# Kernel optimization log

Hardware: AMD Instinct MI355X
Metric: run time of the kernel (lower is better)

## Reference

```python
import jax, jax.numpy as jnp
import numpy as np

B, T, D, H, d = 2, 2048, 1024, 16, 64
INNER = H * d
SCALE = d ** -0.5


def _rope(x, inv_freq):
    # x: [B, H, T, d], interleaved rotary as in the torch module
    t = x.shape[2]
    pos = jnp.arange(t, dtype=jnp.float32)
    freqs = pos[:, None] * inv_freq[None, :]          # [T, d/2]
    cos_f, sin_f = jnp.cos(freqs), jnp.sin(freqs)
    x1, x2 = x[..., 0::2], x[..., 1::2]
    y1 = x1 * cos_f - x2 * sin_f
    y2 = x1 * sin_f + x2 * cos_f
    return jnp.stack([y1, y2], axis=-1).reshape(x.shape)


def setup_inputs() -> dict:
    key = jax.random.key(0)
    ks = jax.random.split(key, 6)
    x = jax.random.normal(ks[0], (B, T, D), jnp.float32)
    W_qkv = jax.random.normal(ks[1], (D, 3 * INNER), jnp.float32) * (D ** -0.5)
    W_out = jax.random.normal(ks[2], (INNER, D), jnp.float32) * (INNER ** -0.5)
    W_dt = jax.random.normal(ks[3], (D, H), jnp.float32) * 0.01
    b_dt = jnp.full((H,), -4.0, jnp.float32)
    W_gsp = jax.random.normal(ks[4], (D, INNER), jnp.float32) * 0.01
    b_gsp = jnp.full((INNER,), -3.0, jnp.float32)
    inv_freq = 1.0 / (10000.0 ** (jnp.arange(0, d, 2, dtype=jnp.float32) / d))
    return {"x": x, "W_qkv": W_qkv, "W_out": W_out, "W_dt": W_dt,
            "b_dt": b_dt, "W_gsp": W_gsp, "b_gsp": b_gsp, "inv_freq": inv_freq}


def reference(x, W_qkv, W_out, W_dt, b_dt, W_gsp, b_gsp, inv_freq):
    qkv = (x @ W_qkv).reshape(B, T, 3, H, d)
    Q = jnp.moveaxis(qkv[:, :, 0], 1, 2)   # [B,H,T,d]
    K = jnp.moveaxis(qkv[:, :, 1], 1, 2)
    V = jnp.moveaxis(qkv[:, :, 2], 1, 2)
    Q = _rope(Q, inv_freq)
    K = _rope(K, inv_freq)

    dt = jax.nn.softplus(x @ W_dt + b_dt)             # [B,T,H]
    gamma = jnp.moveaxis(jnp.exp(-dt), 1, 2)          # [B,H,T]

    p = jax.nn.sigmoid(x @ W_gsp + b_gsp).reshape(B, T, H, d)
    p = jnp.moveaxis(p, 1, 2)                          # [B,H,T,d]
    gamma_eff = gamma[..., None] * (1.0 - p) + p
    gamma_scalar = gamma_eff.mean(axis=-1)            # [B,H,T]
    V = V * (1.0 - p)

    log_gamma = jnp.log(jnp.clip(gamma_scalar, 1e-6, 1.0 - 1e-6))
    lgc = jnp.cumsum(log_gamma, axis=-1)              # [B,H,T]
    log_D = jnp.clip(lgc[..., :, None] - lgc[..., None, :], -20.0, 0.0)
    causal = jnp.tril(jnp.ones((T, T), jnp.float32))
    Dm = jnp.exp(log_D) * causal                      # [B,H,T,T]

    Wscore = jnp.einsum('bhtd,bhsd->bhts', Q * SCALE, K)
    A = Wscore * Dm
    Y = jnp.einsum('bhts,bhsd->bhtd', A, V)
    Y = jnp.moveaxis(Y, 1, 2).reshape(B, T, INNER)
    return Y @ W_out
```

## Files before the change

kernel.cpp:

```cpp
#include <hip/hip_runtime.h>
#include <hip/hip_bf16.h>
#include <math.h>

#define B_     2
#define T_     2048
#define D_     1024
#define H_     16
#define INNER_ 1024
#define NC_    4096
#define SCALE_ 0.125f

typedef unsigned short u16;
typedef short short8 __attribute__((ext_vector_type(8)));
typedef float f32x4 __attribute__((ext_vector_type(4)));
typedef float f32x16 __attribute__((ext_vector_type(16)));
typedef unsigned short u16x4 __attribute__((ext_vector_type(4)));
typedef unsigned int u32x2 __attribute__((ext_vector_type(2)));

__device__ __forceinline__ u16 f2bf(float x) {
  union { float f; unsigned u; } v; v.f = x;
  unsigned r = v.u + 0x7fffu + ((v.u >> 16) & 1u);
  return (u16)(r >> 16);
}
__device__ __forceinline__ float b2f(u16 x) {
  union { unsigned u; float f; } v; v.u = ((unsigned)x) << 16;
  return v.f;
}
__device__ __forceinline__ unsigned cvtpk(float lo, float hi) {
  unsigned r;
  asm("v_cvt_pk_bf16_f32 %0, %1, %2" : "=v"(r) : "v"(lo), "v"(hi));
  return r;
}
__device__ __forceinline__ void gload16(const void* g, void* l) {
  __builtin_amdgcn_global_load_lds(
      (const __attribute__((address_space(1))) void*)g,
      (__attribute__((address_space(3))) void*)l, 16, 0, 0);
}

__global__ __launch_bounds__(256) void prep_kernel(
    const float* __restrict__ x, const float* __restrict__ W_qkv,
    const float* __restrict__ W_gsp, const float* __restrict__ W_out,
    const float* __restrict__ W_dt, const float* __restrict__ inv_freq,
    u16* __restrict__ xb, u16* __restrict__ Wcombt, u16* __restrict__ Woutt,
    u16* __restrict__ Wdtb, float2* __restrict__ tab) {
  const int bid = blockIdx.x, tid = threadIdx.x;
  if (bid < 1280) {
    const float* src; u16* dst; int N, nx, ky;
    if (bid < 768)       { src = W_qkv; dst = Wcombt;                N = 3072; nx = bid % 48;          ky = bid / 48; }
    else if (bid < 1024) { src = W_gsp; dst = Wcombt + 3072 * 1024;  N = 1024; nx = (bid - 768) % 16;  ky = (bid - 768) / 16; }
    else                 { src = W_out; dst = Woutt;                 N = 1024; nx = (bid - 1024) % 16; ky = (bid - 1024) / 16; }
    __shared__ float tile[64][65];
    const int k0 = ky * 64, n0 = nx * 64;
    for (int e = tid; e < 4096; e += 256) {
      int kk = e >> 6, nn = e & 63;
      tile[kk][nn] = src[(size_t)(k0 + kk) * N + n0 + nn];
    }
    __syncthreads();
    for (int e = tid; e < 4096; e += 256) {
      int nn = e >> 6, kk = e & 63;
      dst[(size_t)(n0 + nn) * 1024 + k0 + kk] = f2bf(tile[kk][nn]);
    }
  } else if (bid < 1344) {
    int i = (bid - 1280) * 256 + tid;
    int k = i >> 4, h = i & 15;
    Wdtb[(size_t)h * D_ + k] = f2bf(W_dt[i]);
  } else if (bid < 1600) {
    int i = (bid - 1344) * 256 + tid;
    int t = i >> 5, j = i & 31;
    float s, c;
    sincosf((float)t * inv_freq[j], &s, &c);
    tab[i] = make_float2(c, s);
  } else {
    int base = (bid - 1600) * 1024 + tid;
#pragma unroll
    for (int r = 0; r < 4; ++r) {
      int i = base + r * 256;
      float4 v = *reinterpret_cast<const float4*>(x + (size_t)i * 4);
      u16x4 o; o.x = f2bf(v.x); o.y = f2bf(v.y); o.z = f2bf(v.z); o.w = f2bf(v.w);
      *reinterpret_cast<u16x4*>(xb + (size_t)i * 4) = o;
    }
  }
}

__global__ __launch_bounds__(256, 2) void gemm_big(
    const u16* __restrict__ A, const u16* __restrict__ Bt,
    u16* __restrict__ C) {
  __shared__ u16 As[2][128 * 32] __attribute__((aligned(16)));
  __shared__ u16 Bs[2][256 * 32] __attribute__((aligned(16)));
  const int tid = threadIdx.x;
  const int w = tid >> 6, l = tid & 63;
  const int bid = blockIdx.x;
  const int xcd = bid & 7, idx = bid >> 3;
  const int brow = xcd * 4 + (idx & 3);
  const int bcol = idx >> 2;
  const int m0 = brow * 128, n0 = bcol * 256;
  const int ql = l & 15, g4 = l >> 4;
  const int srow = tid >> 2;
  const int ssl  = (tid & 3) ^ (srow & 3);

  const u16* Ag = A + (size_t)m0 * D_;
  const u16* Bg = Bt + (size_t)n0 * D_;

  auto STAGE = [&](int kt, int bp) {
#pragma unroll
    for (int c = 0; c < 2; ++c)
      gload16(Ag + (size_t)(c * 64 + srow) * D_ + kt * 32 + ssl * 8,
              (char*)As[bp] + c * 4096 + tid * 16);
#pragma unroll
    for (int c = 0; c < 4; ++c)
      gload16(Bg + (size_t)(c * 64 + srow) * D_ + kt * 32 + ssl * 8,
              (char*)Bs[bp] + c * 4096 + tid * 16);
  };

  f32x4 acc[8][4] = {};
  STAGE(0, 0);

  const int NT = D_ / 32;
  for (int kt = 0; kt < NT; ++kt) {
    const int bp = kt & 1;
    asm volatile("s_waitcnt vmcnt(0)" ::: "memory");
    __builtin_amdgcn_sched_barrier(0);
    __builtin_amdgcn_s_barrier();
    __builtin_amdgcn_sched_barrier(0);
    if (kt + 1 < NT) STAGE(kt + 1, bp ^ 1);

    const char* Asb = (const char*)As[bp];
    const char* Bsb = (const char*)Bs[bp];
    short8 bf[4], af[4];
#pragma unroll
    for (int nf = 0; nf < 4; ++nf) {
      int row = w * 64 + nf * 16 + ql;
      bf[nf] = *(const short8*)(Bsb + row * 64 + ((g4 ^ (row & 3)) << 4));
    }
#pragma unroll
    for (int mf = 0; mf < 4; ++mf) {
      int row = mf * 16 + ql;
      af[mf] = *(const short8*)(Asb + row * 64 + ((g4 ^ (row & 3)) << 4));
    }
    __builtin_amdgcn_s_setprio(1);
#pragma unroll
    for (int mf = 0; mf < 4; ++mf)
#pragma unroll
      for (int nf = 0; nf < 4; ++nf)
        acc[mf][nf] = __builtin_amdgcn_mfma_f32_16x16x32_bf16(af[mf], bf[nf], acc[mf][nf], 0, 0, 0);
    __builtin_amdgcn_s_setprio(0);
#pragma unroll
    for (int mf = 0; mf < 4; ++mf) {
      int row = 64 + mf * 16 + ql;
      af[mf] = *(const short8*)(Asb + row * 64 + ((g4 ^ (row & 3)) << 4));
    }
    __builtin_amdgcn_s_setprio(1);
#pragma unroll
    for (int mf = 0; mf < 4; ++mf)
#pragma unroll
      for (int nf = 0; nf < 4; ++nf)
        acc[mf + 4][nf] = __builtin_amdgcn_mfma_f32_16x16x32_bf16(af[mf], bf[nf], acc[mf + 4][nf], 0, 0, 0);
    __builtin_amdgcn_s_setprio(0);
  }

#pragma unroll
  for (int mf = 0; mf < 8; ++mf) {
#pragma unroll
    for (int r = 0; r < 4; ++r) {
      size_t row = (size_t)(m0 + mf * 16 + g4 * 4 + r);
      size_t base = row * NC_ + n0 + w * 64 + ql;
#pragma unroll
      for (int nf = 0; nf < 4; ++nf)
        C[base + nf * 16] = f2bf(acc[mf][nf][r]);
    }
  }
}

template <bool BF16OUT>
__global__ __launch_bounds__(256) void gemm_bt(
    const u16* __restrict__ A, const u16* __restrict__ Bt,
    void* __restrict__ Cv, int M, int N, int K) {
  __shared__ u16 As[2][128 * 64] __attribute__((aligned(16)));
  __shared__ u16 Bs[2][128 * 64] __attribute__((aligned(16)));
  const int tid = threadIdx.x, w = tid >> 6, l = tid & 63;
  const int rpx = (M >> 7) >> 3;
  const int bid = blockIdx.x;
  const int xcd = bid & 7, idx = bid >> 3;
  const int brow = xcd * rpx + (idx % rpx);
  const int bcol = idx / rpx;
  const int m0 = brow * 128, n0 = bcol * 128;
  const int wr = (w >> 1) * 64, wc = (w & 1) * 64;
  const int srow = l >> 3;
  const int kgrp = ((l & 7) ^ srow) * 8;

  f32x4 acc[4][4] = {};

  auto stage = [&](int kt, int bs) {
#pragma unroll
    for (int i = 0; i < 4; ++i) {
      int c = w * 4 + i;
      int row = c * 8 + srow;
      gload16(A + (size_t)(m0 + row) * K + kt * 64 + kgrp, (char*)As[bs] + c * 1024);
      gload16(Bt + (size_t)(n0 + row) * K + kt * 64 + kgrp, (char*)Bs[bs] + c * 1024);
    }
  };

  stage(0, 0);
  const int NT = K >> 6;
  for (int kt = 0; kt < NT; ++kt) {
    asm volatile("s_waitcnt vmcnt(0)" ::: "memory");
    __builtin_amdgcn_sched_barrier(0);
    __builtin_amdgcn_s_barrier();
    __builtin_amdgcn_sched_barrier(0);
    if (kt + 1 < NT) stage(kt + 1, (kt + 1) & 1);

    const char* Asb = (const char*)As[kt & 1];
    const char* Bsb = (const char*)Bs[kt & 1];
#pragma unroll
    for (int kk = 0; kk < 2; ++kk) {
      short8 af[4], bf[4];
#pragma unroll
      for (int i = 0; i < 4; ++i) {
        int ra = wr + i * 16 + (l & 15);
        int sa = kk * 4 + (l >> 4);
        af[i] = *(const short8*)(Asb + ra * 128 + ((sa ^ (ra & 7)) << 4));
        int rb = wc + i * 16 + (l & 15);
        bf[i] = *(const short8*)(Bsb + rb * 128 + ((sa ^ (rb & 7)) << 4));
      }
#pragma unroll
      for (int i = 0; i < 4; ++i)
#pragma unroll
        for (int j = 0; j < 4; ++j)
          acc[i][j] = __builtin_amdgcn_mfma_f32_16x16x32_bf16(af[i], bf[j], acc[i][j], 0, 0, 0);
    }
  }
#pragma unroll
  for (int i = 0; i < 4; ++i) {
#pragma unroll
    for (int r = 0; r < 4; ++r) {
      size_t row = (size_t)(m0 + wr + i * 16 + (l >> 4) * 4 + r);
      size_t base = row * N + n0 + wc + (l & 15);
#pragma unroll
      for (int j = 0; j < 4; ++j) {
        if (BF16OUT) ((u16*)Cv)[base + j * 16] = f2bf(acc[i][j][r]);
        else         ((float*)Cv)[base + j * 16] = acc[i][j][r];
      }
    }
  }
}

__global__ __launch_bounds__(256) void pointwise_kernel(
    const u16* __restrict__ C, const u16* __restrict__ xb,
    const u16* __restrict__ Wdtb, const float* __restrict__ b_dt,
    const float* __restrict__ b_gsp, const float2* __restrict__ tab,
    u16* __restrict__ Qb, u16* __restrict__ Kb, u16* __restrict__ Vb,
    float* __restrict__ lg) {
  const int row = blockIdx.x * 4 + (threadIdx.x >> 6);
  const int l = threadIdx.x & 63;
  const int b = row >> 11, t = row & (T_ - 1);
  const int h = l >> 2;
  const int dd0 = (l & 3) * 16;
  const int col = h * 64 + dd0;
  const size_t cb = (size_t)row * NC_;

  float gsum = 0.f;
  {
    const int kc = (l & 3) * 256;
    const short8* xpg = (const short8*)(xb + (size_t)row * D_ + kc);
    const short8* wpg = (const short8*)(Wdtb + h * D_ + kc);
#pragma unroll
    for (int i = 0; i < 32; ++i) {
      short8 xv = xpg[i], wv = wpg[i];
#pragma unroll
      for (int j = 0; j < 8; ++j) gsum += b2f((u16)xv[j]) * b2f((u16)wv[j]);
    }
    gsum += __shfl_xor(gsum, 1);
    gsum += __shfl_xor(gsum, 2);
  }
  const float dtv = gsum + b_dt[h];
  const float sp = (dtv > 20.f) ? dtv : log1pf(__expf(dtv));
  const float gh = __expf(-sp);

  const short8* qp = (const short8*)(C + cb + col);
  const short8* kp = (const short8*)(C + cb + 1024 + col);
  const short8* vp = (const short8*)(C + cb + 2048 + col);
  const short8* pp = (const short8*)(C + cb + 3072 + col);
  short8 q0 = qp[0], q1 = qp[1];
  short8 k0 = kp[0], k1 = kp[1];
  short8 v0 = vp[0], v1 = vp[1];
  short8 pr0 = pp[0], pr1 = pp[1];

  float ge = 0.f;
  short8 vo0, vo1;
#pragma unroll
  for (int i = 0; i < 8; ++i) {
    float pv = b2f((u16)pr0[i]) + b_gsp[col + i];
    float p = 1.f / (1.f + __expf(-pv));
    ge += gh * (1.f - p) + p;
    vo0[i] = (short)f2bf(b2f((u16)v0[i]) * (1.f - p));
    float pv1 = b2f((u16)pr1[i]) + b_gsp[col + 8 + i];
    float p1 = 1.f / (1.f + __expf(-pv1));
    ge += gh * (1.f - p1) + p1;
    vo1[i] = (short)f2bf(b2f((u16)v1[i]) * (1.f - p1));
  }
  const size_t hm = (((size_t)(b * H_ + h)) * T_ + t) * 64 + dd0;
  ((short8*)(Vb + hm))[0] = vo0;
  ((short8*)(Vb + hm))[1] = vo1;

  ge += __shfl_xor(ge, 1);
  ge += __shfl_xor(ge, 2);
  if ((l & 3) == 0) {
    float gs = ge * (1.f / 64.f);
    gs = fminf(fmaxf(gs, 1e-6f), 1.f - 1e-6f);
    lg[((size_t)(b * H_ + h)) * T_ + t] = logf(gs);
  }

  short8 qo0, qo1, ko0, ko1;
  const float2* cs = tab + t * 32 + (dd0 >> 1);
#pragma unroll
  for (int m = 0; m < 4; ++m) {
    float2 c0 = cs[m];
    float qa = b2f((u16)q0[2 * m]), qb = b2f((u16)q0[2 * m + 1]);
    qo0[2 * m]     = (short)f2bf((qa * c0.x - qb * c0.y) * SCALE_);
    qo0[2 * m + 1] = (short)f2bf((qa * c0.y + qb * c0.x) * SCALE_);
    float ka = b2f((u16)k0[2 * m]), kb = b2f((u16)k0[2 * m + 1]);
    ko0[2 * m]     = (short)f2bf(ka * c0.x - kb * c0.y);
    ko0[2 * m + 1] = (short)f2bf(ka * c0.y + kb * c0.x);
    float2 c1 = cs[4 + m];
    float qa1 = b2f((u16)q1[2 * m]), qb1 = b2f((u16)q1[2 * m + 1]);
    qo1[2 * m]     = (short)f2bf((qa1 * c1.x - qb1 * c1.y) * SCALE_);
    qo1[2 * m + 1] = (short)f2bf((qa1 * c1.y + qb1 * c1.x) * SCALE_);
    float ka1 = b2f((u16)k1[2 * m]), kb1 = b2f((u16)k1[2 * m + 1]);
    ko1[2 * m]     = (short)f2bf(ka1 * c1.x - kb1 * c1.y);
    ko1[2 * m + 1] = (short)f2bf(ka1 * c1.y + kb1 * c1.x);
  }
  ((short8*)(Qb + hm))[0] = qo0; ((short8*)(Qb + hm))[1] = qo1;
  ((short8*)(Kb + hm))[0] = ko0; ((short8*)(Kb + hm))[1] = ko1;
}

__global__ __launch_bounds__(256) void scan_kernel(
    const float* __restrict__ lg, float* __restrict__ lgc) {
  const size_t base = (size_t)blockIdx.x * T_;
  const int tid = threadIdx.x;
  __shared__ float sums[256];
  float loc[8];
  float run = 0.f;
#pragma unroll
  for (int i = 0; i < 8; ++i) { run += lg[base + tid * 8 + i]; loc[i] = run; }
  sums[tid] = run;
  __syncthreads();
  if (tid == 0) {
    float r = 0.f;
    for (int i = 0; i < 256; ++i) { float v = sums[i]; sums[i] = r; r += v; }
  }
  __syncthreads();
  const float off = sums[tid];
#pragma unroll
  for (int i = 0; i < 8; ++i) lgc[base + tid * 8 + i] = off + loc[i];
}

__global__ __launch_bounds__(256) void kv_prep_kernel(
    const u16* __restrict__ Vb, const float* __restrict__ lgc,
    u16* __restrict__ Vtg) {
  const int stile = blockIdx.x;
  const int bh = blockIdx.y;
  const int tid = threadIdx.x;
  __shared__ u16 vt[64][72];
  const size_t base = ((size_t)bh * T_ + (size_t)stile * 64) * 64;
  const float* lgp = lgc + (size_t)bh * T_;
  const float lgb = lgp[stile * 64];
#pragma unroll
  for (int i = 0; i < 2; ++i) {
    int c = tid * 2 + i;
    int row = c >> 3, k8 = (c & 7) * 8;
    float beta = __expf(lgb - lgp[stile * 64 + row]);
    short8 vv = *(const short8*)(Vb + base + row * 64 + k8);
#pragma unroll
    for (int j = 0; j < 8; ++j) vt[row][k8 + j] = f2bf(b2f((u16)vv[j]) * beta);
  }
  __syncthreads();
#pragma unroll
  for (int i = 0; i < 2; ++i) {
    int c = tid * 2 + i;
    int dd = c >> 3, t8 = (c & 7) * 8;
    short8 o;
#pragma unroll
    for (int j = 0; j < 8; ++j) o[j] = (short)vt[t8 + j][dd];
    *(short8*)(Vtg + ((size_t)(bh * 32 + stile) * 64 + dd) * 64 + t8) = o;
  }
}

__global__ __launch_bounds__(256) void attn_mfma(
    const u16* __restrict__ Qb, const u16* __restrict__ Kb,
    const u16* __restrict__ Vtg, const float* __restrict__ lgc,
    u16* __restrict__ Y) {
  const int i = blockIdx.x;
  const int xcd = i & 7;
  const int half = i >> 8;
  const int r = (i >> 3) & 31;
  const int q8 = r >> 2;
  const int bh_hi = r & 3;
  const int qb = half ? (15 - q8) : q8;
  const int bh = xcd + (bh_hi << 3);
  const int b = bh >> 4, h = bh & 15;
  const int tid = threadIdx.x, w = tid >> 6, l = tid & 63;
  const int l31 = l & 31, hi = l >> 5;
  __shared__ u16 Ks[3][64 * 64] __attribute__((aligned(16)));
  __shared__ u16 Vs[3][64 * 64] __attribute__((aligned(16)));
  const u16* Qg = Qb + (size_t)bh * T_ * 64;
  const u16* Kg = Kb + (size_t)bh * T_ * 64;
  const u16* Vg = Vtg + (size_t)bh * 32 * 4096;
  const float* lgp = lgc + (size_t)bh * T_;
  const int srow = l >> 3, slot8 = l & 7;

  const int q0 = qb * 128 + w * 32;
  const int qg = q0 + l31;
  short8 qf[4];
#pragma unroll
  for (int kk = 0; kk < 4; ++kk)
    qf[kk] = *(const short8*)(Qg + (size_t)qg * 64 + kk * 16 + hi * 8);
  const float lgq = lgp[qg];
  const float lgtop = lgp[qb * 128];

  f32x16 yacc0 = {}, yacc1 = {};

  const int st0 = qb * 2 + 1;
  int s_min;
  {
    int lo = 0, hic = st0;
    while (lo < hic) {
      int mid = (lo + hic) >> 1;
      if (lgtop - lgp[mid * 64 + 63] > -20.f) hic = mid; else lo = mid + 1;
    }
    s_min = lo;
  }

  auto STAGE = [&](int s) {
    const int bs = s % 3;
#pragma unroll
    for (int i2 = 0; i2 < 2; ++i2) {
      int c = w * 2 + i2, row = c * 8 + srow;
      int kg = (slot8 ^ (row & 7)) * 8;
      gload16(Kg + (size_t)(s * 64 + row) * 64 + kg, (char*)Ks[bs] + c * 1024);
      gload16(Vg + (size_t)s * 4096 + row * 64 + kg, (char*)Vs[bs] + c * 1024);
    }
  };

  STAGE(st0);
  if (st0 - 1 >= s_min) STAGE(st0 - 1);

  for (int st = st0; st >= s_min; --st) {
    if (st - 1 >= s_min) asm volatile("s_waitcnt vmcnt(4)" ::: "memory");
    else                 asm volatile("s_waitcnt vmcnt(0)" ::: "memory");
    __builtin_amdgcn_sched_barrier(0);
    __builtin_amdgcn_s_barrier();
    __builtin_amdgcn_sched_barrier(0);
    if (st - 2 >= s_min) STAGE(st - 2);

    const bool allinv = (st * 64 > q0 + 31);
    if (!allinv) {
      const int bs = st % 3;
      const char* Ksb = (const char*)Ks[bs];
      const char* Vsb = (const char*)Vs[bs];
      const float alpha = __expf(lgq - lgp[st * 64]);
      const bool domask = (st * 64 + 63 > q0);
      const int qrel = qg - st * 64;
#pragma unroll
      for (int sblk = 0; sblk < 2; ++sblk) {
        f32x16 c = {};
        __builtin_amdgcn_s_setprio(1);
#pragma unroll
        for (int kk = 0; kk < 4; ++kk) {
          int row = sblk * 32 + l31;
          short8 kf = *(const short8*)(Ksb + row * 128 + (((kk * 2 + hi) ^ (row & 7)) << 4));
          c = __builtin_amdgcn_mfma_f32_32x32x16_bf16(kf, qf[kk], c, 0, 0, 0);
        }
        __builtin_amdgcn_s_setprio(0);
        float pv[16];
#pragma unroll
        for (int ii = 0; ii < 16; ++ii) {
          float p = c[ii] * alpha;
          if (domask) {
            int s64 = sblk * 32 + (ii & 3) + 8 * (ii >> 2) + 4 * hi;
            if (s64 > qrel) p = 0.f;
          }
          pv[ii] = p;
        }
        unsigned A0 = cvtpk(pv[0], pv[1]),  A1 = cvtpk(pv[2], pv[3]);
        unsigned B0 = cvtpk(pv[4], pv[5]),  B1 = cvtpk(pv[6], pv[7]);
        u32x2 ra = __builtin_amdgcn_permlane32_swap(A0, B0, false, false);
        u32x2 rb = __builtin_amdgcn_permlane32_swap(A1, B1, false, false);
        unsigned C0 = cvtpk(pv[8], pv[9]),  C1 = cvtpk(pv[10], pv[11]);
        unsigned D0 = cvtpk(pv[12], pv[13]), D1 = cvtpk(pv[14], pv[15]);
        u32x2 rc = __builtin_amdgcn_permlane32_swap(C0, D0, false, false);
        u32x2 rd = __builtin_amdgcn_permlane32_swap(C1, D1, false, false);
        union { unsigned u[4]; short8 s; } f0, f1;
        f0.u[0] = ra[0]; f0.u[1] = rb[0]; f0.u[2] = ra[1]; f0.u[3] = rb[1];
        f1.u[0] = rc[0]; f1.u[1] = rd[0]; f1.u[2] = rc[1]; f1.u[3] = rd[1];
#pragma unroll
        for (int fi = 0; fi < 2; ++fi) {
          const short8 pf = fi ? f1.s : f0.s;
          const int kkg = sblk * 2 + fi;
          short8 vf0 = *(const short8*)(Vsb + l31 * 128 + (((kkg * 2 + hi) ^ (l31 & 7)) << 4));
          short8 vf1 = *(const short8*)(Vsb + (32 + l31) * 128 + (((kkg * 2 + hi) ^ (l31 & 7)) << 4));
          __builtin_amdgcn_s_setprio(1);
          yacc0 = __builtin_amdgcn_mfma_f32_32x32x16_bf16(pf, vf0, yacc0, 0, 0, 0);
          yacc1 = __builtin_amdgcn_mfma_f32_32x32x16_bf16(pf, vf1, yacc1, 0, 0, 0);
          __builtin_amdgcn_s_setprio(0);
        }
      }
    }
  }

#pragma unroll
  for (int reg = 0; reg < 16; ++reg) {
    int qrow = (reg & 3) + 8 * (reg >> 2) + 4 * hi;
    size_t rowg = (size_t)(b * T_) + qb * 128 + w * 32 + qrow;
    Y[rowg * INNER_ + h * 64 + l31] = f2bf(yacc0[reg]);
    Y[rowg * INNER_ + h * 64 + 32 + l31] = f2bf(yacc1[reg]);
  }
}

extern "C" void kernel_launch(void* const* d_in, const int* in_sizes, int n_in,
                              void* d_out, int out_size, void* d_ws, size_t ws_size,
                              hipStream_t stream) {
  const float* x        = (const float*)d_in[0];
  const float* W_qkv    = (const float*)d_in[1];
  const float* W_out    = (const float*)d_in[2];
  const float* W_dt     = (const float*)d_in[3];
  const float* b_dt     = (const float*)d_in[4];
  const float* W_gsp    = (const float*)d_in[5];
  const float* b_gsp    = (const float*)d_in[6];
  const float* inv_freq = (const float*)d_in[7];
  float* out = (float*)d_out;

  const int M = B_ * T_;
  char* p = (char*)d_ws;
  auto alloc = [&](size_t bytes) {
    char* r = p; p += (bytes + 255) & ~(size_t)255; return r;
  };
  u16*    xb    = (u16*)alloc((size_t)M * D_ * 2);
  u16*    Wcombt= (u16*)alloc((size_t)NC_ * D_ * 2);
  u16*    Woutt = (u16*)alloc((size_t)D_ * INNER_ * 2);
  u16*    Wdtb  = (u16*)alloc((size_t)H_ * D_ * 2);
  u16*    Cqkvp = (u16*)alloc((size_t)M * NC_ * 2);
  u16*    Qb    = (u16*)alloc((size_t)B_ * H_ * T_ * 64 * 2);
  u16*    Kb    = (u16*)alloc((size_t)B_ * H_ * T_ * 64 * 2);
  u16*    Vb    = (u16*)alloc((size_t)B_ * H_ * T_ * 64 * 2);
  float*  lg    = (float*)alloc((size_t)B_ * H_ * T_ * 4);
  float*  lgc   = (float*)alloc((size_t)B_ * H_ * T_ * 4);
  float2* tab   = (float2*)alloc((size_t)T_ * 32 * 8);
  u16*    Vtg   = Cqkvp;
  u16*    Yb    = Cqkvp + (size_t)4 * 1024 * 1024;

  prep_kernel<<<2624, 256, 0, stream>>>(x, W_qkv, W_gsp, W_out, W_dt, inv_freq,
                                        xb, Wcombt, Woutt, Wdtb, tab);
  gemm_big<<<512, 256, 0, stream>>>(xb, Wcombt, Cqkvp);

  pointwise_kernel<<<M / 4, 256, 0, stream>>>(Cqkvp, xb, Wdtb, b_dt, b_gsp,
                                              tab, Qb, Kb, Vb, lg);
  scan_kernel<<<B_ * H_, 256, 0, stream>>>(lg, lgc);
  kv_prep_kernel<<<dim3(T_ / 64, B_ * H_), 256, 0, stream>>>(Vb, lgc, Vtg);

  attn_mfma<<<512, 256, 0, stream>>>(Qb, Kb, Vtg, lgc, Yb);

  gemm_bt<false><<<256, 256, 0, stream>>>(Yb, Woutt, out, M, D_, INNER_);
}
```

Measured before the change: 150.6 us.

## Restructure attention into 512-thread blocks with 256-row query tiles and split-S reduction

The attention kernel now runs 256 blocks of 512 threads. Each block covers 256 query rows, and each wave handles 64 query rows over half of each 64-key tile. The two key halves are combined at the end through an LDS reduction. This reuses K fragments across two query sub-tiles and halves the number of K/V tile loads per query, but it drops the old reversed query-block ordering used for causal load balancing and adds barriers and a reduction step. Per-block work is now more uneven and fewer blocks are in flight.

```diff
diff --git a/kernel.cpp b/kernel.cpp
--- a/kernel.cpp
+++ b/kernel.cpp
@@ -385,41 +385,40 @@
   }
 }
 
-__global__ __launch_bounds__(256) void attn_mfma(
+__global__ __launch_bounds__(512) void attn_mfma(
     const u16* __restrict__ Qb, const u16* __restrict__ Kb,
     const u16* __restrict__ Vtg, const float* __restrict__ lgc,
     u16* __restrict__ Y) {
   const int i = blockIdx.x;
   const int xcd = i & 7;
-  const int half = i >> 8;
-  const int r = (i >> 3) & 31;
-  const int q8 = r >> 2;
-  const int bh_hi = r & 3;
-  const int qb = half ? (15 - q8) : q8;
-  const int bh = xcd + (bh_hi << 3);
+  const int rr = i >> 3;
+  const int qb = rr & 7;
+  const int bh = xcd + ((rr >> 3) << 3);
   const int b = bh >> 4, h = bh & 15;
   const int tid = threadIdx.x, w = tid >> 6, l = tid & 63;
+  const int wq = w & 3, ws = w >> 2;
   const int l31 = l & 31, hi = l >> 5;
-  __shared__ u16 Ks[3][64 * 64] __attribute__((aligned(16)));
-  __shared__ u16 Vs[3][64 * 64] __attribute__((aligned(16)));
+  __shared__ char smem[3 * 16384] __attribute__((aligned(16)));
   const u16* Qg = Qb + (size_t)bh * T_ * 64;
   const u16* Kg = Kb + (size_t)bh * T_ * 64;
   const u16* Vg = Vtg + (size_t)bh * 32 * 4096;
   const float* lgp = lgc + (size_t)bh * T_;
   const int srow = l >> 3, slot8 = l & 7;
 
-  const int q0 = qb * 128 + w * 32;
-  const int qg = q0 + l31;
-  short8 qf[4];
-#pragma unroll
-  for (int kk = 0; kk < 4; ++kk)
-    qf[kk] = *(const short8*)(Qg + (size_t)qg * 64 + kk * 16 + hi * 8);
-  const float lgq = lgp[qg];
-  const float lgtop = lgp[qb * 128];
-
-  f32x16 yacc0 = {}, yacc1 = {};
-
-  const int st0 = qb * 2 + 1;
+  const int q0w = qb * 256 + wq * 64;
+  const int qg0 = q0w + l31, qg1 = q0w + 32 + l31;
+  short8 qf0[4], qf1[4];
+#pragma unroll
+  for (int kk = 0; kk < 4; ++kk) {
+    qf0[kk] = *(const short8*)(Qg + (size_t)qg0 * 64 + kk * 16 + hi * 8);
+    qf1[kk] = *(const short8*)(Qg + (size_t)qg1 * 64 + kk * 16 + hi * 8);
+  }
+  const float lgq0 = lgp[qg0], lgq1 = lgp[qg1];
+  const float lgtop = lgp[qb * 256];
+
+  f32x16 yacc00 = {}, yacc01 = {}, yacc10 = {}, yacc11 = {};
+
+  const int st0 = qb * 4 + 3;
   int s_min;
   {
     int lo = 0, hic = st0;
@@ -431,88 +430,122 @@
   }
 
   auto STAGE = [&](int s) {
-    const int bs = s % 3;
-#pragma unroll
-    for (int i2 = 0; i2 < 2; ++i2) {
-      int c = w * 2 + i2, row = c * 8 + srow;
-      int kg = (slot8 ^ (row & 7)) * 8;
-      gload16(Kg + (size_t)(s * 64 + row) * 64 + kg, (char*)Ks[bs] + c * 1024);
-      gload16(Vg + (size_t)s * 4096 + row * 64 + kg, (char*)Vs[bs] + c * 1024);
-    }
+    char* base = smem + (s % 3) * 16384;
+    int row = w * 8 + srow;
+    int kg = (slot8 ^ (row & 7)) * 8;
+    gload16(Kg + (size_t)(s * 64 + row) * 64 + kg, base + w * 1024);
+    gload16(Vg + (size_t)s * 4096 + row * 64 + kg, base + 8192 + w * 1024);
   };
 
   STAGE(st0);
   if (st0 - 1 >= s_min) STAGE(st0 - 1);
 
   for (int st = st0; st >= s_min; --st) {
-    if (st - 1 >= s_min) asm volatile("s_waitcnt vmcnt(4)" ::: "memory");
+    if (st - 1 >= s_min) asm volatile("s_waitcnt vmcnt(2)" ::: "memory");
     else                 asm volatile("s_waitcnt vmcnt(0)" ::: "memory");
     __builtin_amdgcn_sched_barrier(0);
     __builtin_amdgcn_s_barrier();
     __builtin_amdgcn_sched_barrier(0);
     if (st - 2 >= s_min) STAGE(st - 2);
 
-    const bool allinv = (st * 64 > q0 + 31);
+    const bool allinv = (st * 64 > q0w + 63);
     if (!allinv) {
-      const int bs = st % 3;
-      const char* Ksb = (const char*)Ks[bs];
-      const char* Vsb = (const char*)Vs[bs];
-      const float alpha = __expf(lgq - lgp[st * 64]);
-      const bool domask = (st * 64 + 63 > q0);
-      const int qrel = qg - st * 64;
-#pragma unroll
-      for (int sblk = 0; sblk < 2; ++sblk) {
-        f32x16 c = {};
-        __builtin_amdgcn_s_setprio(1);
-#pragma unroll
-        for (int kk = 0; kk < 4; ++kk) {
-          int row = sblk * 32 + l31;
-          short8 kf = *(const short8*)(Ksb + row * 128 + (((kk * 2 + hi) ^ (row & 7)) << 4));
-          c = __builtin_amdgcn_mfma_f32_32x32x16_bf16(kf, qf[kk], c, 0, 0, 0);
-        }
-        __builtin_amdgcn_s_setprio(0);
-        float pv[16];
-#pragma unroll
-        for (int ii = 0; ii < 16; ++ii) {
-          float p = c[ii] * alpha;
-          if (domask) {
-            int s64 = sblk * 32 + (ii & 3) + 8 * (ii >> 2) + 4 * hi;
-            if (s64 > qrel) p = 0.f;
-          }
-          pv[ii] = p;
-        }
-        unsigned A0 = cvtpk(pv[0], pv[1]),  A1 = cvtpk(pv[2], pv[3]);
-        unsigned B0 = cvtpk(pv[4], pv[5]),  B1 = cvtpk(pv[6], pv[7]);
-        u32x2 ra = __builtin_amdgcn_permlane32_swap(A0, B0, false, false);
-        u32x2 rb = __builtin_amdgcn_permlane32_swap(A1, B1, false, false);
-        unsigned C0 = cvtpk(pv[8], pv[9]),  C1 = cvtpk(pv[10], pv[11]);
-        unsigned D0 = cvtpk(pv[12], pv[13]), D1 = cvtpk(pv[14], pv[15]);
-        u32x2 rc = __builtin_amdgcn_permlane32_swap(C0, D0, false, false);
-        u32x2 rd = __builtin_amdgcn_permlane32_swap(C1, D1, false, false);
-        union { unsigned u[4]; short8 s; } f0, f1;
-        f0.u[0] = ra[0]; f0.u[1] = rb[0]; f0.u[2] = ra[1]; f0.u[3] = rb[1];
-        f1.u[0] = rc[0]; f1.u[1] = rd[0]; f1.u[2] = rc[1]; f1.u[3] = rd[1];
-#pragma unroll
-        for (int fi = 0; fi < 2; ++fi) {
-          const short8 pf = fi ? f1.s : f0.s;
-          const int kkg = sblk * 2 + fi;
-          short8 vf0 = *(const short8*)(Vsb + l31 * 128 + (((kkg * 2 + hi) ^ (l31 & 7)) << 4));
-          short8 vf1 = *(const short8*)(Vsb + (32 + l31) * 128 + (((kkg * 2 + hi) ^ (l31 & 7)) << 4));
-          __builtin_amdgcn_s_setprio(1);
-          yacc0 = __builtin_amdgcn_mfma_f32_32x32x16_bf16(pf, vf0, yacc0, 0, 0, 0);
-          yacc1 = __builtin_amdgcn_mfma_f32_32x32x16_bf16(pf, vf1, yacc1, 0, 0, 0);
-          __builtin_amdgcn_s_setprio(0);
-        }
+      const char* Ksb = smem + (st % 3) * 16384;
+      const char* Vsb = Ksb + 8192;
+      const float alpha0 = __expf(lgq0 - lgp[st * 64]);
+      const float alpha1 = __expf(lgq1 - lgp[st * 64]);
+      const bool domask = (st * 64 + 63 > q0w);
+      const int qrel0 = qg0 - st * 64, qrel1 = qg1 - st * 64;
+
+      short8 kf[4];
+#pragma unroll
+      for (int kk = 0; kk < 4; ++kk) {
+        int row = ws * 32 + l31;
+        kf[kk] = *(const short8*)(Ksb + row * 128 + (((kk * 2 + hi) ^ (row & 7)) << 4));
       }
-    }
-  }
-
-#pragma unroll
-  for (int reg = 0; reg < 16; ++reg) {
-    int qrow = (reg & 3) + 8 * (reg >> 2) + 4 * hi;
-    size_t rowg = (size_t)(b * T_) + qb * 128 + w * 32 + qrow;
-    Y[rowg * INNER_ + h * 64 + l31] = f2bf(yacc0[reg]);
-    Y[rowg * INNER_ + h * 64 + 32 + l31] = f2bf(yacc1[reg]);
+      f32x16 c0 = {}, c1 = {};
+      __builtin_amdgcn_s_setprio(1);
+#pragma unroll
+      for (int kk = 0; kk < 4; ++kk) {
+        c0 = __builtin_amdgcn_mfma_f32_32x32x16_bf16(kf[kk], qf0[kk], c0, 0, 0, 0);
+        c1 = __builtin_amdgcn_mfma_f32_32x32x16_bf16(kf[kk], qf1[kk], c1, 0, 0, 0);
+      }
+      __builtin_amdgcn_s_setprio(0);
+
+      short8 vf00, vf01, vf10, vf11;
+      {
+        int r0 = l31, r1 = 32 + l31;
+        int k0g = (ws * 2 + 0) * 2 + hi, k1g = (ws * 2 + 1) * 2 + hi;
+        vf00 = *(const short8*)(Vsb + r0 * 128 + ((k0g ^ (r0 & 7)) << 4));
+        vf01 = *(const short8*)(Vsb + r1 * 128 + ((k0g ^ (r1 & 7)) << 4));
+        vf10 = *(const short8*)(Vsb + r0 * 128 + ((k1g ^ (r0 & 7)) << 4));
+        vf11 = *(const short8*)(Vsb + r1 * 128 + ((k1g ^ (r1 & 7)) << 4));
+      }
+
+#define PACK_PV(CC, ALPHA, QREL, YA, YB)                                        \
+      {                                                                          \
+        float pv[16];                                                            \
+        _Pragma("unroll")                                                        \
+        for (int ii = 0; ii < 16; ++ii) {                                        \
+          float p = (CC)[ii] * (ALPHA);                                          \
+          if (domask) {                                                          \
+            int s64 = ws * 32 + (ii & 3) + 8 * (ii >> 2) + 4 * hi;               \
+            if (s64 > (QREL)) p = 0.f;                                           \
+          }                                                                      \
+          pv[ii] = p;                                                            \
+        }                                                                        \
+        unsigned A0 = cvtpk(pv[0], pv[1]),  A1 = cvtpk(pv[2], pv[3]);            \
+        unsigned B0 = cvtpk(pv[4], pv[5]),  B1 = cvtpk(pv[6], pv[7]);            \
+        u32x2 ra = __builtin_amdgcn_permlane32_swap(A0, B0, false, false);       \
+        u32x2 rb = __builtin_amdgcn_permlane32_swap(A1, B1, false, false);       \
+        unsigned C0 = cvtpk(pv[8], pv[9]),  C1 = cvtpk(pv[10], pv[11]);          \
+        unsigned D0 = cvtpk(pv[12], pv[13]), D1 = cvtpk(pv[14], pv[15]);         \
+        u32x2 rc = __builtin_amdgcn_permlane32_swap(C0, D0, false, false);       \
+        u32x2 rd = __builtin_amdgcn_permlane32_swap(C1, D1, false, false);       \
+        union { unsigned u[4]; short8 s; } f0, f1;                               \
+        f0.u[0] = ra[0]; f0.u[1] = rb[0]; f0.u[2] = ra[1]; f0.u[3] = rb[1];      \
+        f1.u[0] = rc[0]; f1.u[1] = rd[0]; f1.u[2] = rc[1]; f1.u[3] = rd[1];      \
+        __builtin_amdgcn_s_setprio(1);                                           \
+        YA = __builtin_amdgcn_mfma_f32_32x32x16_bf16(f0.s, vf00, YA, 0, 0, 0);   \
+        YB = __builtin_amdgcn_mfma_f32_32x32x16_bf16(f0.s, vf01, YB, 0, 0, 0);   \
+        YA = __builtin_amdgcn_mfma_f32_32x32x16_bf16(f1.s, vf10, YA, 0, 0, 0);   \
+        YB = __builtin_amdgcn_mfma_f32_32x32x16_bf16(f1.s, vf11, YB, 0, 0, 0);   \
+        __builtin_amdgcn_s_setprio(0);                                           \
+      }
+      PACK_PV(c0, alpha0, qrel0, yacc00, yacc01)
+      PACK_PV(c1, alpha1, qrel1, yacc10, yacc11)
+#undef PACK_PV
+    }
+  }
+
+#define REDUCE(YA, YB)                                                           \
+  {                                                                              \
+    __syncthreads();                                                             \
+    if (ws == 1) {                                                               \
+      *(f32x16*)(smem + wq * 8192 + l * 128)      = YA;                          \
+      *(f32x16*)(smem + wq * 8192 + l * 128 + 64) = YB;                          \
+    }                                                                            \
+    __syncthreads();                                                             \
+    if (ws == 0) {                                                               \
+      YA += *(const f32x16*)(smem + wq * 8192 + l * 128);                        \
+      YB += *(const f32x16*)(smem + wq * 8192 + l * 128 + 64);                   \
+    }                                                                            \
+  }
+  REDUCE(yacc00, yacc01)
+  REDUCE(yacc10, yacc11)
+#undef REDUCE
+
+  if (ws == 0) {
+#pragma unroll
+    for (int reg = 0; reg < 16; ++reg) {
+      int qrow = (reg & 3) + 8 * (reg >> 2) + 4 * hi;
+      size_t r0 = (size_t)(b * T_) + q0w + qrow;
+      size_t r1 = r0 + 32;
+      Y[r0 * INNER_ + h * 64 + l31]      = f2bf(yacc00[reg]);
+      Y[r0 * INNER_ + h * 64 + 32 + l31] = f2bf(yacc01[reg]);
+      Y[r1 * INNER_ + h * 64 + l31]      = f2bf(yacc10[reg]);
+      Y[r1 * INNER_ + h * 64 + 32 + l31] = f2bf(yacc11[reg]);
+    }
   }
 }
 
@@ -557,7 +590,7 @@
   scan_kernel<<<B_ * H_, 256, 0, stream>>>(lg, lgc);
   kv_prep_kernel<<<dim3(T_ / 64, B_ * H_), 256, 0, stream>>>(Vb, lgc, Vtg);
 
-  attn_mfma<<<512, 256, 0, stream>>>(Qb, Kb, Vtg, lgc, Yb);
+  attn_mfma<<<256, 512, 0, stream>>>(Qb, Kb, Vtg, lgc, Yb);
 
   gemm_bt<false><<<256, 256, 0, stream>>>(Yb, Woutt, out, M, D_, INNER_);
 }
```

Result: no change. 153.4 us (+1.9%).
